# Performance work log

Measured on AMD Instinct MI355X. Metric: run time of the kernel, lower is better.

## Reference

```python
import jax, jax.numpy as jnp
import numpy as np

D = 64          # d_model
H = 128         # ffn_hidden_dim
N = 10000       # nodes
E = 50000       # edges
NEG_SLOPE = 0.01  # LeakyReLU default


def setup_inputs() -> dict:
    key = jax.random.key(0)
    ks = jax.random.split(key, 10)
    x = jax.random.normal(ks[0], (N, D), dtype=jnp.float32)
    edge_index = jax.random.randint(ks[1], (2, E), 0, N)
    edge_attr = jax.random.normal(ks[2], (E, D), dtype=jnp.float32)
    # MapE2NxN params (stored as [in, out] so forward is x @ W + b)
    w1 = jax.random.normal(ks[3], (D, H), dtype=jnp.float32) / np.sqrt(D)
    b1 = jnp.zeros((H,), dtype=jnp.float32)
    w2 = jax.random.normal(ks[4], (H, D * D), dtype=jnp.float32) / np.sqrt(H)
    b2 = jnp.zeros((D * D,), dtype=jnp.float32)
    # NNConv root weight + bias
    root = jax.random.normal(ks[5], (D, D), dtype=jnp.float32) / np.sqrt(D)
    bias = jnp.zeros((D,), dtype=jnp.float32)
    # LayerNorm affine params
    gamma = jnp.ones((D,), dtype=jnp.float32)
    beta = jnp.zeros((D,), dtype=jnp.float32)
    return {"x": x, "edge_attr": edge_attr, "gamma": gamma, "beta": beta,
            "w1": w1, "b1": b1, "w2": w2, "b2": b2,
            "root": root, "bias": bias, "edge_index": edge_index}


def _layer_norm(h, gamma, beta, eps=1e-5):
    mu = jnp.mean(h, axis=-1, keepdims=True)
    var = jnp.var(h, axis=-1, keepdims=True)
    return (h - mu) * jax.lax.rsqrt(var + eps) * gamma + beta


def _leaky_relu(h):
    return jnp.where(h >= 0, h, NEG_SLOPE * h)


def reference(x, edge_attr, gamma, beta, w1, b1, w2, b2, root, bias, edge_index):
    src, dst = edge_index[0], edge_index[1]
    # DeepGCNLayer block='res+': pre-activation norm -> act -> (dropout p=0) -> conv -> residual
    h = _leaky_relu(_layer_norm(x, gamma, beta))
    # MapE2NxN on edge attributes -> per-edge [D, D] weight matrix
    we = _leaky_relu(edge_attr @ w1 + b1) @ w2 + b2   # [E, D*D]
    we = we.reshape(E, D, D)
    # per-edge matvec with source node features (PyG NNConv message)
    msg = jnp.einsum('ed,edf->ef', h[src], we)        # [E, D]
    # scatter-mean aggregate into destination nodes
    agg = jax.ops.segment_sum(msg, dst, num_segments=N)
    cnt = jax.ops.segment_sum(jnp.ones((E,), dtype=msg.dtype), dst, num_segments=N)
    agg = agg / jnp.maximum(cnt, 1.0)[:, None]
    # root transform + bias, then residual
    out = agg + h @ root + bias
    return x + out
```

## Files before the change

kernel.cpp:

```cpp
#include <hip/hip_runtime.h>

#define NS 10000
#define DD 64
#define HH 128
#define EE 50000
#define SLOPE 0.01f
#define BPAD 8448

typedef __attribute__((ext_vector_type(8))) short short8;
typedef __attribute__((ext_vector_type(8))) _Float16 half8;
typedef __attribute__((ext_vector_type(4))) float f32x4;

static __device__ __forceinline__ unsigned short f2bf(float f) {
  unsigned int u = __float_as_uint(f);
  u += 0x7fff + ((u >> 16) & 1);
  return (unsigned short)(u >> 16);
}
static __device__ __forceinline__ unsigned short f2h(float f) {
  _Float16 v = (_Float16)f;
  return __builtin_bit_cast(unsigned short, v);
}
static __device__ __forceinline__ unsigned pkmul(unsigned a, unsigned b) {
  unsigned r;
  asm("v_pk_mul_f16 %0, %1, %2" : "=v"(r) : "v"(a), "v"(b));
  return r;
}
static __device__ __forceinline__ unsigned duplo(unsigned v) {
  v &= 0xffffu; return v | (v << 16);
}
static __device__ __forceinline__ unsigned duphi(unsigned v) {
  v >>= 16; return v | (v << 16);
}

__device__ __forceinline__ float wave_sum64(float v) {
  #pragma unroll
  for (int m = 32; m >= 1; m >>= 1) v += __shfl_xor(v, m, 64);
  return v;
}

#define TBLK 128
#define PBLK 2500
#define UB 782
__global__ __launch_bounds__(256) void k_prep(const float* __restrict__ x,
    const float* __restrict__ gamma, const float* __restrict__ beta,
    float* __restrict__ h, unsigned short* __restrict__ h16,
    const float* __restrict__ ea, const float* __restrict__ w2,
    unsigned short* __restrict__ w2e, const float* __restrict__ w1,
    const float* __restrict__ b1, unsigned short* __restrict__ u16,
    const float* __restrict__ b2, const int* __restrict__ ei,
    int* __restrict__ cntdst) {
  __shared__ __align__(16) unsigned char smem[18432];
  int t = threadIdx.x;
  int bid = blockIdx.x;
  if (bid < TBLK) {
    float (*tile)[65] = (float(*)[65])smem;
    int k = bid;
    #pragma unroll
    for (int i = 0; i < 16; ++i) {
      int idx = t + i * 256;
      tile[idx >> 6][idx & 63] = w2[k * (DD * DD) + idx];
    }
    __syncthreads();
    #pragma unroll
    for (int it = 0; it < 2; ++it) {
      int slot = t + it * 256;
      int f = slot >> 3, l8 = slot & 7;
      short8 o;
      #pragma unroll
      for (int j = 0; j < 8; ++j) o[j] = f2h(tile[l8 * 8 + j][f]);
      *(short8*)(w2e + (size_t)f * BPAD + k * DD + l8 * 8) = o;
    }
    return;
  }
  if (bid == TBLK) {
    #pragma unroll
    for (int i = 0; i < 16; ++i) {
      int idx = t + i * 256;
      int d = idx >> 6, f = idx & 63;
      w2e[(size_t)f * BPAD + 8192 + d] = f2h(b2[idx]);
    }
    #pragma unroll
    for (int i = 0; i < 6; ++i) {
      int slot = t + i * 256;
      int f = slot / 24, z8 = slot % 24;
      short8 z = {};
      *(short8*)(w2e + (size_t)f * BPAD + 8256 + z8 * 8) = z;
    }
    return;
  }
  if (bid < TBLK + 1 + PBLK) {
    int pbid = bid - TBLK - 1;
    int gid = pbid * 256 + t;
    if (gid < EE) atomicAdd(&cntdst[ei[EE + gid]], 1);
    int wid = t >> 6;
    int lane = t & 63;
    int row = pbid * 4 + wid;
    if (row >= NS) return;
    float v = x[row * DD + lane];
    float s = wave_sum64(v);
    float s2 = wave_sum64(v * v);
    float mu = s * (1.0f / 64.0f);
    float var = s2 * (1.0f / 64.0f) - mu * mu;
    float r = rsqrtf(var + 1e-5f);
    float hn = (v - mu) * r * gamma[lane] + beta[lane];
    float hv = hn >= 0.f ? hn : SLOPE * hn;
    h[row * DD + lane] = hv;
    h16[row * DD + lane] = f2h(hv);
    return;
  }
  int ublk = bid - TBLK - 1 - PBLK;
  unsigned short (*W)[72] = (unsigned short(*)[72])smem;
  int w = t >> 6, lane = t & 63, lr = lane & 15, lg = lane >> 4;
  int r0 = ublk * 64 + w * 16;
  int ra = r0 + lr; if (ra >= EE) ra = EE - 1;
  const float* ep = ea + (size_t)ra * DD;
  float4 e0 = *(const float4*)(ep + lg * 8);
  float4 e1 = *(const float4*)(ep + lg * 8 + 4);
  float4 e2 = *(const float4*)(ep + 32 + lg * 8);
  float4 e3 = *(const float4*)(ep + 32 + lg * 8 + 4);
  #pragma unroll
  for (int i = 0; i < 32; ++i) {
    int idx = t + i * 256;
    int d = idx >> 7, hc = idx & 127;
    W[hc][d] = f2bf(w1[idx]);
  }
  __syncthreads();
  short8 a0, a1;
  a0[0] = f2bf(e0.x); a0[1] = f2bf(e0.y); a0[2] = f2bf(e0.z); a0[3] = f2bf(e0.w);
  a0[4] = f2bf(e1.x); a0[5] = f2bf(e1.y); a0[6] = f2bf(e1.z); a0[7] = f2bf(e1.w);
  a1[0] = f2bf(e2.x); a1[1] = f2bf(e2.y); a1[2] = f2bf(e2.z); a1[3] = f2bf(e2.w);
  a1[4] = f2bf(e3.x); a1[5] = f2bf(e3.y); a1[6] = f2bf(e3.z); a1[7] = f2bf(e3.w);
  short8 bb0[8], bb1[8];
  #pragma unroll
  for (int ni = 0; ni < 8; ++ni) {
    bb0[ni] = *(const short8*)(&W[ni * 16 + lr][lg * 8]);
    bb1[ni] = *(const short8*)(&W[ni * 16 + lr][32 + lg * 8]);
  }
  f32x4 acc[8] = {};
  #pragma unroll
  for (int ni = 0; ni < 8; ++ni) {
    acc[ni] = __builtin_amdgcn_mfma_f32_16x16x32_bf16(a0, bb0[ni], acc[ni], 0, 0, 0);
    acc[ni] = __builtin_amdgcn_mfma_f32_16x16x32_bf16(a1, bb1[ni], acc[ni], 0, 0, 0);
  }
  #pragma unroll
  for (int ni = 0; ni < 8; ++ni) {
    int col = ni * 16 + lr;
    float bb = b1[col];
    #pragma unroll
    for (int reg = 0; reg < 4; ++reg) {
      int gr = r0 + lg * 4 + reg;
      if (gr < EE) {
        float vv = acc[ni][reg] + bb;
        u16[(size_t)gr * HH + col] = f2h(vv >= 0.f ? vv : SLOPE * vv);
      }
    }
  }
}

__global__ __launch_bounds__(256) void k_msgd(
    const unsigned short* __restrict__ u16, const unsigned short* __restrict__ h16,
    const unsigned short* __restrict__ w2e, const int* __restrict__ ei,
    float* __restrict__ agg) {
  __shared__ unsigned short Bs[64 * 256];
  int t = threadIdx.x;
  int w = t >> 6, lane = t & 63, lr = lane & 15, lg = lane >> 4;
  int cq = blockIdx.y;
  int nch = (cq == 3) ? 9 : 8;
  int ebase = (blockIdx.x * 4 + w) * 32;
  int e0 = ebase + lr, e1 = ebase + 16 + lr;
  int e0c = e0 < EE ? e0 : EE - 1;
  int e1c = e1 < EE ? e1 : EE - 1;
  int s0 = ei[e0c], s1 = ei[e1c];
  unsigned hp0[2][4], hp1[2][4];
  #pragma unroll
  for (int par = 0; par < 2; ++par) {
    uint4 v0 = *(const uint4*)(h16 + (size_t)s0 * DD + par * 32 + lg * 8);
    uint4 v1 = *(const uint4*)(h16 + (size_t)s1 * DD + par * 32 + lg * 8);
    hp0[par][0] = v0.x; hp0[par][1] = v0.y; hp0[par][2] = v0.z; hp0[par][3] = v0.w;
    hp1[par][0] = v1.x; hp1[par][1] = v1.y; hp1[par][2] = v1.z; hp1[par][3] = v1.w;
  }
  union { uint4 q[4]; unsigned s[16]; } ub0, ub1;
  {
    const unsigned short* p0 = u16 + (size_t)e0c * HH + cq * 32;
    const unsigned short* p1 = u16 + (size_t)e1c * HH + cq * 32;
    #pragma unroll
    for (int i = 0; i < 4; ++i) {
      ub0.q[i] = *(const uint4*)(p0 + i * 8);
      ub1.q[i] = *(const uint4*)(p1 + i * 8);
    }
  }
  int sf = t >> 4, so8 = t & 15;
  short8 sreg[8];
  {
    int ch0 = cq * 8;
    #pragma unroll
    for (int i = 0; i < 8; ++i) {
      int f = sf + (i & 3) * 16;
      int o8 = so8 + (i >> 2) * 16;
      sreg[i] = *(const short8*)(w2e + (size_t)f * BPAD + ch0 * 256 + o8 * 8);
    }
  }
  f32x4 acc[2][4] = {};
  for (int ci = 0; ci < nch; ++ci) {
    if (ci) __syncthreads();
    #pragma unroll
    for (int i = 0; i < 8; ++i) {
      int f = sf + (i & 3) * 16;
      int o8 = so8 + (i >> 2) * 16;
      *(short8*)(&Bs[f * 256 + (o8 ^ (f & 7)) * 8]) = sreg[i];
    }
    __syncthreads();
    if (ci + 1 < nch) {
      int ch2 = (ci + 1 < 8) ? (cq * 8 + ci + 1) : 32;
      #pragma unroll
      for (int i = 0; i < 8; ++i) {
        int f = sf + (i & 3) * 16;
        int o8 = so8 + (i >> 2) * 16;
        sreg[i] = *(const short8*)(w2e + (size_t)f * BPAD + ch2 * 256 + o8 * 8);
      }
    }
    unsigned ud0[4], ud1[4];
    if (ci < 8) {
      ud0[0] = duplo(ub0.s[ci * 2]);     ud0[1] = duphi(ub0.s[ci * 2]);
      ud0[2] = duplo(ub0.s[ci * 2 + 1]); ud0[3] = duphi(ub0.s[ci * 2 + 1]);
      ud1[0] = duplo(ub1.s[ci * 2]);     ud1[1] = duphi(ub1.s[ci * 2]);
      ud1[2] = duplo(ub1.s[ci * 2 + 1]); ud1[3] = duphi(ub1.s[ci * 2 + 1]);
    } else {
      ud0[0] = 0x3C003C00u; ud0[1] = 0u; ud0[2] = 0u; ud0[3] = 0u;
      ud1[0] = 0x3C003C00u; ud1[1] = 0u; ud1[2] = 0u; ud1[3] = 0u;
    }
    #pragma unroll
    for (int ks = 0; ks < 8; ++ks) {
      int par = ks & 1, kk = ks >> 1;
      union { unsigned u[4]; half8 h; } pa0, pa1;
      #pragma unroll
      for (int jj = 0; jj < 4; ++jj) {
        pa0.u[jj] = pkmul(kk == 0 ? ud0[0] : kk == 1 ? ud0[1] : kk == 2 ? ud0[2] : ud0[3],
                          hp0[par][jj]);
        pa1.u[jj] = pkmul(kk == 0 ? ud1[0] : kk == 1 ? ud1[1] : kk == 2 ? ud1[2] : ud1[3],
                          hp1[par][jj]);
      }
      int o8r = ks * 4 + lg;
      #pragma unroll
      for (int ft = 0; ft < 4; ++ft) {
        int f = ft * 16 + lr;
        half8 b = *(const half8*)(&Bs[f * 256 + (o8r ^ (f & 7)) * 8]);
        acc[0][ft] = __builtin_amdgcn_mfma_f32_16x16x32_f16(pa0.h, b,
                                                            acc[0][ft], 0, 0, 0);
        acc[1][ft] = __builtin_amdgcn_mfma_f32_16x16x32_f16(pa1.h, b,
                                                            acc[1][ft], 0, 0, 0);
      }
    }
  }
  #pragma unroll
  for (int m = 0; m < 2; ++m)
    #pragma unroll
    for (int reg = 0; reg < 4; ++reg) {
      int ee = ebase + m * 16 + lg * 4 + reg;
      if (ee < EE) {
        int dstn = ei[EE + ee];
        #pragma unroll
        for (int ft = 0; ft < 4; ++ft)
          atomicAdd(&agg[(size_t)dstn * DD + ft * 16 + lr],
                    m == 0 ? acc[0][ft][reg] : acc[1][ft][reg]);
      }
    }
}

__global__ __launch_bounds__(256) void k_final(const float* __restrict__ x,
    const float* __restrict__ h, const float* __restrict__ root,
    const float* __restrict__ bias, const float* __restrict__ agg,
    const int* __restrict__ cnt, float* __restrict__ out) {
  __shared__ float Bs[DD][DD + 1];
  __shared__ float As[32][DD];
  int t = threadIdx.x;
  #pragma unroll
  for (int i = 0; i < 16; ++i) {
    int idx = t + i * 256;
    Bs[idx >> 6][idx & 63] = root[idx];
  }
  int row0 = blockIdx.x * 32;
  #pragma unroll
  for (int i = 0; i < 8; ++i) {
    int idx = t + i * 256;
    int r = idx >> 6, d = idx & 63;
    int gr = row0 + r;
    As[r][d] = (gr < NS) ? h[gr * DD + d] : 0.f;
  }
  __syncthreads();
  int r = t >> 3;
  int c0 = (t & 7) * 8;
  int gr = row0 + r;
  if (gr >= NS) return;
  float acc[8] = {};
  for (int d = 0; d < DD; ++d) {
    float a = As[r][d];
    #pragma unroll
    for (int j = 0; j < 8; ++j) acc[j] += a * Bs[d][c0 + j];
  }
  float inv = 1.0f / fmaxf((float)cnt[gr], 1.0f);
  #pragma unroll
  for (int j = 0; j < 8; ++j) {
    size_t gi = (size_t)gr * DD + c0 + j;
    out[gi] = x[gi] + agg[gi] * inv + acc[j] + bias[c0 + j];
  }
}

extern "C" void kernel_launch(void* const* d_in, const int* in_sizes, int n_in,
                              void* d_out, int out_size, void* d_ws, size_t ws_size,
                              hipStream_t stream) {
  const float* x     = (const float*)d_in[0];
  const float* ea    = (const float*)d_in[1];
  const float* gamma = (const float*)d_in[2];
  const float* beta  = (const float*)d_in[3];
  const float* w1    = (const float*)d_in[4];
  const float* b1    = (const float*)d_in[5];
  const float* w2    = (const float*)d_in[6];
  const float* b2    = (const float*)d_in[7];
  const float* root  = (const float*)d_in[8];
  const float* bias  = (const float*)d_in[9];
  const int*   ei    = (const int*)d_in[10];
  float* out = (float*)d_out;

  char* p = (char*)d_ws;
  auto carve = [&](size_t bytes) {
    char* q = p;
    p += (bytes + 255) & ~(size_t)255;
    return q;
  };
  float* h            = (float*)carve(sizeof(float) * NS * DD);
  unsigned short* h16 = (unsigned short*)carve(sizeof(short) * NS * DD);
  unsigned short* w2e = (unsigned short*)carve(sizeof(short) * (size_t)DD * BPAD);
  unsigned short* u16 = (unsigned short*)carve(sizeof(short) * (size_t)EE * HH);
  char* z0 = p;
  float* agg          = (float*)carve(sizeof(float) * NS * DD);
  int* cntdst         = (int*)carve(sizeof(int) * NS);
  size_t zlen = (size_t)(p - z0);

  (void)hipMemsetAsync(z0, 0, zlen, stream);
  k_prep<<<dim3(TBLK + 1 + PBLK + UB), dim3(256), 0, stream>>>(
      x, gamma, beta, h, h16, ea, w2, w2e, w1, b1, u16, b2, ei, cntdst);
  k_msgd<<<dim3((EE + 127) / 128, 4), dim3(256), 0, stream>>>(
      u16, h16, w2e, ei, agg);
  k_final<<<dim3((NS + 31) / 32), dim3(256), 0, stream>>>(x, h, root, bias, agg,
                                                          cntdst, out);
}
```

Measured before the change: 119.2 us.

## Double-buffer w2 tiles in LDS with smaller chunks in message kernel

Splits the per-edge weight (w2) staging into 16 half-size chunks per block and double-buffers them in shared memory. The next chunk is written to the alternate buffer while MFMAs run on the current one, so each chunk needs one barrier instead of two. The global prefetch runs two chunks ahead through registers. This needs fewer sreg registers but runs twice as many loop iterations, adding more barriers and smaller MFMA batches per barrier.

New measurement: 121.6 us. 1.02x slower.

```diff
diff --git a/kernel.cpp b/kernel.cpp
--- a/kernel.cpp
+++ b/kernel.cpp
@@ -161,11 +161,10 @@
     const unsigned short* __restrict__ u16, const unsigned short* __restrict__ h16,
     const unsigned short* __restrict__ w2e, const int* __restrict__ ei,
     float* __restrict__ agg) {
-  __shared__ unsigned short Bs[64 * 256];
+  __shared__ unsigned short Bs[2][64 * 128];
   int t = threadIdx.x;
   int w = t >> 6, lane = t & 63, lr = lane & 15, lg = lane >> 4;
   int cq = blockIdx.y;
-  int nch = (cq == 3) ? 9 : 8;
   int ebase = (blockIdx.x * 4 + w) * 32;
   int e0 = ebase + lr, e1 = ebase + 16 + lr;
   int e0c = e0 < EE ? e0 : EE - 1;
@@ -189,68 +188,66 @@
       ub1.q[i] = *(const uint4*)(p1 + i * 8);
     }
   }
-  int sf = t >> 4, so8 = t & 15;
-  short8 sreg[8];
-  {
-    int ch0 = cq * 8;
-    #pragma unroll
-    for (int i = 0; i < 8; ++i) {
-      int f = sf + (i & 3) * 16;
-      int o8 = so8 + (i >> 2) * 16;
-      sreg[i] = *(const short8*)(w2e + (size_t)f * BPAD + ch0 * 256 + o8 * 8);
-    }
-  }
+  short8 sreg[4];
+  auto issue = [&](int ch) {
+    #pragma unroll
+    for (int i = 0; i < 4; ++i) {
+      int slot = t + i * 256;
+      int f = slot >> 4, o8 = slot & 15;
+      sreg[i] = *(const short8*)(w2e + (size_t)f * BPAD + ch * 128 + o8 * 8);
+    }
+  };
+  auto wrbuf = [&](int b) {
+    #pragma unroll
+    for (int i = 0; i < 4; ++i) {
+      int slot = t + i * 256;
+      int f = slot >> 4, o8 = slot & 15;
+      *(short8*)(&Bs[b][f * 128 + (o8 ^ (f & 7)) * 8]) = sreg[i];
+    }
+  };
   f32x4 acc[2][4] = {};
-  for (int ci = 0; ci < nch; ++ci) {
-    if (ci) __syncthreads();
-    #pragma unroll
-    for (int i = 0; i < 8; ++i) {
-      int f = sf + (i & 3) * 16;
-      int o8 = so8 + (i >> 2) * 16;
-      *(short8*)(&Bs[f * 256 + (o8 ^ (f & 7)) * 8]) = sreg[i];
-    }
-    __syncthreads();
-    if (ci + 1 < nch) {
-      int ch2 = (ci + 1 < 8) ? (cq * 8 + ci + 1) : 32;
-      #pragma unroll
-      for (int i = 0; i < 8; ++i) {
-        int f = sf + (i & 3) * 16;
-        int o8 = so8 + (i >> 2) * 16;
-        sreg[i] = *(const short8*)(w2e + (size_t)f * BPAD + ch2 * 256 + o8 * 8);
-      }
-    }
-    unsigned ud0[4], ud1[4];
-    if (ci < 8) {
-      ud0[0] = duplo(ub0.s[ci * 2]);     ud0[1] = duphi(ub0.s[ci * 2]);
-      ud0[2] = duplo(ub0.s[ci * 2 + 1]); ud0[3] = duphi(ub0.s[ci * 2 + 1]);
-      ud1[0] = duplo(ub1.s[ci * 2]);     ud1[1] = duphi(ub1.s[ci * 2]);
-      ud1[2] = duplo(ub1.s[ci * 2 + 1]); ud1[3] = duphi(ub1.s[ci * 2 + 1]);
-    } else {
-      ud0[0] = 0x3C003C00u; ud0[1] = 0u; ud0[2] = 0u; ud0[3] = 0u;
-      ud1[0] = 0x3C003C00u; ud1[1] = 0u; ud1[2] = 0u; ud1[3] = 0u;
-    }
-    #pragma unroll
-    for (int ks = 0; ks < 8; ++ks) {
+  auto mfma_block = [&](int cur, unsigned d0l, unsigned d0h,
+                        unsigned d1l, unsigned d1h) {
+    #pragma unroll
+    for (int ks = 0; ks < 4; ++ks) {
       int par = ks & 1, kk = ks >> 1;
+      unsigned s0v = kk ? d0h : d0l;
+      unsigned s1v = kk ? d1h : d1l;
       union { unsigned u[4]; half8 h; } pa0, pa1;
       #pragma unroll
       for (int jj = 0; jj < 4; ++jj) {
-        pa0.u[jj] = pkmul(kk == 0 ? ud0[0] : kk == 1 ? ud0[1] : kk == 2 ? ud0[2] : ud0[3],
-                          hp0[par][jj]);
-        pa1.u[jj] = pkmul(kk == 0 ? ud1[0] : kk == 1 ? ud1[1] : kk == 2 ? ud1[2] : ud1[3],
-                          hp1[par][jj]);
+        pa0.u[jj] = pkmul(s0v, hp0[par][jj]);
+        pa1.u[jj] = pkmul(s1v, hp1[par][jj]);
       }
       int o8r = ks * 4 + lg;
       #pragma unroll
       for (int ft = 0; ft < 4; ++ft) {
         int f = ft * 16 + lr;
-        half8 b = *(const half8*)(&Bs[f * 256 + (o8r ^ (f & 7)) * 8]);
+        half8 b = *(const half8*)(&Bs[cur][f * 128 + ((o8r ^ (f & 7))) * 8]);
         acc[0][ft] = __builtin_amdgcn_mfma_f32_16x16x32_f16(pa0.h, b,
                                                             acc[0][ft], 0, 0, 0);
         acc[1][ft] = __builtin_amdgcn_mfma_f32_16x16x32_f16(pa1.h, b,
                                                             acc[1][ft], 0, 0, 0);
       }
     }
+  };
+  issue(cq * 16 + 0);
+  wrbuf(0);
+  issue(cq * 16 + 1);
+  __syncthreads();
+  #pragma unroll
+  for (int ci = 0; ci < 16; ++ci) {
+    int cur = ci & 1;
+    if (ci < 15) wrbuf(cur ^ 1);
+    else if (cq == 3) wrbuf(cur ^ 1);
+    if (ci < 14) issue(cq * 16 + ci + 2);
+    else if (ci == 14 && cq == 3) issue(64);
+    unsigned u0w = ub0.s[ci], u1w = ub1.s[ci];
+    mfma_block(cur, duplo(u0w), duphi(u0w), duplo(u1w), duphi(u1w));
+    __syncthreads();
+  }
+  if (cq == 3) {
+    mfma_block(0, 0x3C003C00u, 0u, 0x3C003C00u, 0u);
   }
   #pragma unroll
   for (int m = 0; m < 2; ++m)
```
